# Kernel tuning notes

Hardware: AMD Instinct MI355X
Metric: run time of the kernel (lower is better)

## Reference

```python
import jax, jax.numpy as jnp
import numpy as np
from jax import lax

B, C, IC, NH, H, W, HID = 32, 128, 256, 8, 64, 64, 512


def _bn(x, g, b, m, v, eps):
    # inference-mode BatchNorm2d over NCHW
    inv = g / jnp.sqrt(v + eps)
    return x * inv[None, :, None, None] + (b - m * inv)[None, :, None, None]


def setup_inputs() -> dict:
    key = jax.random.key(0)
    ks = jax.random.split(key, 10)
    n = lambda i, shape, s: jax.random.normal(ks[i], shape, jnp.float32) * s
    return {
        "x": n(0, (B, C, H, W), 1.0),
        "bn1_g": jnp.ones((C,), jnp.float32),
        "bn1_b": jnp.zeros((C,), jnp.float32),
        "bn1_m": n(1, (C,), 0.1),
        "bn1_v": jax.random.uniform(ks[2], (C,), jnp.float32, 0.5, 1.5),
        "k": n(3, (IC, C), 0.001),   # torch.randn(...)*0.001, 1x1 kernel flattened
        "v": n(4, (C, IC), 0.001),
        "bn2_g": jnp.ones((C,), jnp.float32),
        "bn2_b": jnp.zeros((C,), jnp.float32),
        "bn2_m": n(5, (C,), 0.1),
        "bn2_v": jax.random.uniform(ks[6], (C,), jnp.float32, 0.5, 1.5),
        "w1": n(7, (HID, C, 3, 3), 0.05),
        "b1": jnp.zeros((HID,), jnp.float32),
        "w2": n(8, (C, HID, 3, 3), 0.05),
        "b2": jnp.zeros((C,), jnp.float32),
    }


def _conv3x3(x, w, b):
    y = lax.conv_general_dilated(x, w, (1, 1), 'SAME',
                                 dimension_numbers=('NCHW', 'OIHW', 'NCHW'))
    return y + b[None, :, None, None]


def reference(x, bn1_g, bn1_b, bn1_m, bn1_v, k, v,
              bn2_g, bn2_b, bn2_m, bn2_v, w1, b1, w2, b2):
    # --- ExternalAttention (use_cross_kv=False, same_in_out_chs -> stride 1) ---
    h = _bn(x, bn1_g, bn1_b, bn1_m, bn1_v, 1e-5)
    h = jnp.einsum('bchw,oc->bohw', h, k)            # 1x1 conv with external k bank
    # double normalization (_act_dn): softmax over spatial, sum-normalize per head-channel
    h = h.reshape(B, NH, IC // NH, H * W)
    h = jax.nn.softmax(h, axis=3)
    h = h / (jnp.sum(h, axis=2, keepdims=True) + 1e-6)
    h = h.reshape(B, IC, H, W)
    h = jnp.einsum('bchw,oc->bohw', h, v)            # 1x1 conv with external v bank
    x = x + h                                        # residual (EABlock wrapper)
    # --- MLP1 (BN eps=1e-6, 3x3 conv, GELU, 3x3 conv; dropout inactive in eval) ---
    m = _bn(x, bn2_g, bn2_b, bn2_m, bn2_v, 1e-6)
    m = _conv3x3(m, w1, b1)
    m = jax.nn.gelu(m, approximate=False)            # torch nn.GELU default = exact erf
    m = _conv3x3(m, w2, b2)
    return x + m
```

## Files before the change

### kernel.cpp

```cpp
#include <hip/hip_runtime.h>
#include <hip/hip_bf16.h>
#include <math.h>


#define Bn 32
#define Cn 128
#define ICn 256
#define NHn 8
#define HWn 4096
#define HIDn 512
#define GPAD 40

typedef __bf16 bf16x8 __attribute__((ext_vector_type(8)));
typedef float f32x4 __attribute__((ext_vector_type(4)));

__device__ __forceinline__ uint32_t bf16r(float v) {
  uint32_t u = __float_as_uint(v);
  return (u + 0x7FFFu + ((u >> 16) & 1u)) >> 16;
}
__device__ __forceinline__ void split_bf16(float v, uint32_t& h, uint32_t& l) {
  h = bf16r(v);
  float rem = v - __uint_as_float(h << 16);
  l = bf16r(rem);
}
__device__ __forceinline__ uint4 pack8(const float* v) {
  uint32_t w[4];
#pragma unroll
  for (int q = 0; q < 4; ++q)
    w[q] = bf16r(v[2 * q]) | (bf16r(v[2 * q + 1]) << 16);
  return make_uint4(w[0], w[1], w[2], w[3]);
}
#define MFMA(a, b, c) __builtin_amdgcn_mfma_f32_16x16x32_bf16((a), (b), (c), 0, 0, 0)

__global__ __launch_bounds__(256) void prep_a_kernel(
    const float* __restrict__ bn1_g, const float* __restrict__ bn1_b,
    const float* __restrict__ bn1_m, const float* __restrict__ bn1_v,
    const float* __restrict__ kmat,
    const float* __restrict__ bn2_g, const float* __restrict__ bn2_b,
    const float* __restrict__ bn2_m, const float* __restrict__ bn2_v,
    float* __restrict__ keff, float* __restrict__ biask,
    float* __restrict__ inv2, float* __restrict__ beta2) {
  __shared__ float sinv1[Cn], sbeta1[Cn];
  const int t = threadIdx.x;
  if (t < Cn) {
    float i1 = bn1_g[t] / sqrtf(bn1_v[t] + 1e-5f);
    sinv1[t] = i1;
    sbeta1[t] = bn1_b[t] - bn1_m[t] * i1;
    float i2 = bn2_g[t] / sqrtf(bn2_v[t] + 1e-6f);
    inv2[t] = i2;
    beta2[t] = bn2_b[t] - bn2_m[t] * i2;
  }
  __syncthreads();
  float bk = 0.f;
  for (int c = 0; c < Cn; ++c) {
    float kv = kmat[t * Cn + c];
    keff[t * Cn + c] = kv * sinv1[c];
    bk += kv * sbeta1[c];
  }
  biask[t] = bk;
}

__global__ __launch_bounds__(256) void prep_b_kernel(
    const float* __restrict__ keff, const float* __restrict__ vmat,
    const float* __restrict__ w1, const float* __restrict__ w2,
    ushort* __restrict__ k1h, ushort* __restrict__ k1l,
    ushort* __restrict__ vh, ushort* __restrict__ vl,
    ushort* __restrict__ wt1h, ushort* __restrict__ wt1l,
    ushort* __restrict__ wt2h, ushort* __restrict__ wt2l) {
  const int stride = gridDim.x * blockDim.x;
  const int tid0 = blockIdx.x * blockDim.x + threadIdx.x;
  uint32_t h, l;
  for (int d = tid0; d < ICn * Cn; d += stride) {
    int e = d & 7, lane = (d >> 3) & 63, f = d >> 9;
    int ib = f & 3, ob = f >> 2;
    int oc = ob * 16 + (lane & 15), k = ib * 32 + (lane >> 4) * 8 + e;
    split_bf16(keff[oc * Cn + k], h, l);
    k1h[d] = (ushort)h; k1l[d] = (ushort)l;
  }
  for (int d = tid0; d < Cn * ICn; d += stride) {
    int e = d & 7, lane = (d >> 3) & 63, f = d >> 9;
    int ib = f & 7, ob = f >> 3;
    int oc = ob * 16 + (lane & 15), k = ib * 32 + (lane >> 4) * 8 + e;
    split_bf16(vmat[oc * ICn + k], h, l);
    vh[d] = (ushort)h; vl[d] = (ushort)l;
  }
  for (int d = tid0; d < 9 * HIDn * Cn; d += stride) {
    int e = d & 7, lane = (d >> 3) & 63, f = d >> 9;
    int ib = f & 3, obt = f >> 2;
    int ob = obt & 31, tap = obt >> 5;
    int oc = ob * 16 + (lane & 15), k = ib * 32 + (lane >> 4) * 8 + e;
    split_bf16(w1[(oc * Cn + k) * 9 + tap], h, l);
    wt1h[d] = (ushort)h; wt1l[d] = (ushort)l;
  }
  for (int d = tid0; d < 9 * Cn * HIDn; d += stride) {
    int e = d & 7, lane = (d >> 3) & 63, f = d >> 9;
    int ib = f & 15, obt = f >> 4;
    int ob = obt & 7, tap = obt >> 3;
    int oc = ob * 16 + (lane & 15), k = ib * 32 + (lane >> 4) * 8 + e;
    split_bf16(w2[(oc * HIDn + k) * 9 + tap], h, l);
    wt2h[d] = (ushort)h; wt2l[d] = (ushort)l;
  }
}

__global__ __launch_bounds__(256, 4) void gemm1_mfma(
    const float* __restrict__ x, const ushort* __restrict__ k1h,
    const ushort* __restrict__ k1l, const float* __restrict__ biask,
    float* __restrict__ S, int b0) {
  const int tid = threadIdx.x, lane = tid & 63, wave = tid >> 6;
  const int wm = wave >> 1, wn = wave & 1;
  const int l15 = lane & 15, lg = lane >> 4;
  const int p0 = blockIdx.x * 128;
  const int oc0 = blockIdx.y * 128;
  const int bg = b0 + blockIdx.z;
  __shared__ __align__(16) ushort Xb[128 * GPAD];
  f32x4 acc[4][4] = {};
  for (int c0 = 0; c0 < Cn; c0 += 32) {
    __syncthreads();
    for (int i = tid; i < 512; i += 256) {
      int p = i & 127, g = i >> 7;
      const float* src = x + ((size_t)bg * Cn + c0 + g * 8) * HWn + p0 + p;
      float v[8];
#pragma unroll
      for (int j = 0; j < 8; ++j) v[j] = src[(size_t)j * HWn];
      *(uint4*)&Xb[p * GPAD + g * 8] = pack8(v);
    }
    __syncthreads();
    bf16x8 Bf[4];
#pragma unroll
    for (int nf = 0; nf < 4; ++nf)
      Bf[nf] = *(const bf16x8*)&Xb[(wn * 64 + nf * 16 + l15) * GPAD + lg * 8];
#pragma unroll
    for (int mf = 0; mf < 4; ++mf) {
      int fidx = ((oc0 >> 4) + wm * 4 + mf) * 4 + (c0 >> 5);
      bf16x8 Ah = *(const bf16x8*)(k1h + (size_t)fidx * 512 + lane * 8);
      bf16x8 Al = *(const bf16x8*)(k1l + (size_t)fidx * 512 + lane * 8);
#pragma unroll
      for (int nf = 0; nf < 4; ++nf)
        acc[mf][nf] = MFMA(Al, Bf[nf], MFMA(Ah, Bf[nf], acc[mf][nf]));
    }
  }
#pragma unroll
  for (int mf = 0; mf < 4; ++mf)
#pragma unroll
    for (int r = 0; r < 4; ++r) {
      int oc = oc0 + wm * 64 + mf * 16 + lg * 4 + r;
      float bk = biask[oc];
#pragma unroll
      for (int nf = 0; nf < 4; ++nf) {
        int p = p0 + wn * 64 + nf * 16 + l15;
        S[((size_t)blockIdx.z * ICn + oc) * HWn + p] = acc[mf][nf][r] + bk;
      }
    }
}

__global__ __launch_bounds__(256) void softmax_kernel(float* __restrict__ S) {
  __shared__ float row[HWn];
  __shared__ float red[4];
  const int t = threadIdx.x;
  float4* rowv = (float4*)row;
  float4* Sv = (float4*)(S + (size_t)blockIdx.x * HWn);
  float lmax = -1e30f;
#pragma unroll
  for (int i = 0; i < 4; ++i) {
    float4 v = Sv[t + 256 * i];
    rowv[t + 256 * i] = v;
    lmax = fmaxf(lmax, fmaxf(fmaxf(v.x, v.y), fmaxf(v.z, v.w)));
  }
#pragma unroll
  for (int off = 32; off; off >>= 1) lmax = fmaxf(lmax, __shfl_xor(lmax, off));
  if ((t & 63) == 0) red[t >> 6] = lmax;
  __syncthreads();
  lmax = fmaxf(fmaxf(red[0], red[1]), fmaxf(red[2], red[3]));
  float lsum = 0.f;
#pragma unroll
  for (int i = 0; i < 4; ++i) {
    float4 v = rowv[t + 256 * i];
    v.x = expf(v.x - lmax); v.y = expf(v.y - lmax);
    v.z = expf(v.z - lmax); v.w = expf(v.w - lmax);
    rowv[t + 256 * i] = v;
    lsum += v.x + v.y + v.z + v.w;
  }
#pragma unroll
  for (int off = 32; off; off >>= 1) lsum += __shfl_xor(lsum, off);
  __syncthreads();
  if ((t & 63) == 0) red[t >> 6] = lsum;
  __syncthreads();
  lsum = red[0] + red[1] + red[2] + red[3];
  float inv = 1.0f / lsum;
#pragma unroll
  for (int i = 0; i < 4; ++i) {
    float4 v = rowv[t + 256 * i];
    v.x *= inv; v.y *= inv; v.z *= inv; v.w *= inv;
    Sv[t + 256 * i] = v;
  }
}

__global__ __launch_bounds__(256) void hsum_kernel(const float* __restrict__ S,
                                                   float* __restrict__ hsum) {
  const int p4 = blockIdx.x * 256 + threadIdx.x;
  const int hh = blockIdx.y, bz = blockIdx.z;
  const float* base = S + ((size_t)bz * ICn + hh * 32) * HWn;
  float4 a = make_float4(0.f, 0.f, 0.f, 0.f);
#pragma unroll
  for (int i = 0; i < 32; ++i) {
    float4 v = ((const float4*)(base + (size_t)i * HWn))[p4];
    a.x += v.x; a.y += v.y; a.z += v.z; a.w += v.w;
  }
  ((float4*)(hsum + ((size_t)bz * NHn + hh) * HWn))[p4] = a;
}

__global__ __launch_bounds__(256, 4) void gemm2_mfma(
    const float* __restrict__ S, const ushort* __restrict__ vh,
    const ushort* __restrict__ vl, const float* __restrict__ hsum,
    const float* __restrict__ x, float* __restrict__ x2, int b0) {
  const int tid = threadIdx.x, lane = tid & 63, wave = tid >> 6;
  const int wm = wave >> 1, wn = wave & 1;
  const int l15 = lane & 15, lg = lane >> 4;
  const int p0 = blockIdx.x * 128;
  const int bz = blockIdx.z, bg = b0 + bz;
  __shared__ __align__(16) ushort Xb[128 * GPAD];
  f32x4 acc[4][4] = {};
  for (int hh = 0; hh < NHn; ++hh) {
    __syncthreads();
    for (int i = tid; i < 512; i += 256) {
      int p = i & 127, g = i >> 7;
      const float* src = S + ((size_t)bz * ICn + hh * 32 + g * 8) * HWn + p0 + p;
      float rr = 1.0f / (hsum[((size_t)bz * NHn + hh) * HWn + p0 + p] + 1e-6f);
      float v[8];
#pragma unroll
      for (int j = 0; j < 8; ++j) v[j] = src[(size_t)j * HWn] * rr;
      *(uint4*)&Xb[p * GPAD + g * 8] = pack8(v);
    }
    __syncthreads();
    bf16x8 Bf[4];
#pragma unroll
    for (int nf = 0; nf < 4; ++nf)
      Bf[nf] = *(const bf16x8*)&Xb[(wn * 64 + nf * 16 + l15) * GPAD + lg * 8];
#pragma unroll
    for (int mf = 0; mf < 4; ++mf) {
      int fidx = (wm * 4 + mf) * 8 + hh;
      bf16x8 Ah = *(const bf16x8*)(vh + (size_t)fidx * 512 + lane * 8);
      bf16x8 Al = *(const bf16x8*)(vl + (size_t)fidx * 512 + lane * 8);
#pragma unroll
      for (int nf = 0; nf < 4; ++nf)
        acc[mf][nf] = MFMA(Al, Bf[nf], MFMA(Ah, Bf[nf], acc[mf][nf]));
    }
  }
#pragma unroll
  for (int mf = 0; mf < 4; ++mf)
#pragma unroll
    for (int r = 0; r < 4; ++r) {
      int c = wm * 64 + mf * 16 + lg * 4 + r;
#pragma unroll
      for (int nf = 0; nf < 4; ++nf) {
        int p = p0 + wn * 64 + nf * 16 + l15;
        size_t off = ((size_t)bg * Cn + c) * HWn + p;
        x2[off] = x[off] + acc[mf][nf][r];
      }
    }
}

template <int IN_C, int OUT_C, bool IN_NHWC, bool DO_BN, bool GELU_NHWC,
          bool DO_RESID, bool IN_ABS, bool OUT_ABS>
__global__ __launch_bounds__(256, 4) void conv_mfma(
    const void* __restrict__ in_v, const ushort* __restrict__ wth,
    const ushort* __restrict__ wtl, const float* __restrict__ bias,
    const float* __restrict__ inv2, const float* __restrict__ beta2,
    const float* __restrict__ resid, void* __restrict__ out_v, int b0) {
  constexpr int NOB = OUT_C / 16, NIB = IN_C / 32;
  const int tid = threadIdx.x, lane = tid & 63, wave = tid >> 6;
  const int wm = wave >> 1, wn = wave & 1;
  const int l15 = lane & 15, lg = lane >> 4;
  const int p0 = blockIdx.x * 128;
  const int y0 = p0 >> 6;
  const int oc0 = blockIdx.y * 128;
  const int bz = blockIdx.z;
  const int bin = IN_ABS ? (b0 + bz) : bz;
  const int bout = OUT_ABS ? (b0 + bz) : bz;
  __shared__ __align__(16) ushort Xb[4 * 66 * GPAD];
  f32x4 acc[4][4] = {};

  for (int ic0 = 0; ic0 < IN_C; ic0 += 32) {
    __syncthreads();
    for (int i = tid; i < 4 * 66 * 4; i += 256) {
      int c = i % 66;
      int rg = i / 66;
      int r = rg & 3, g = rg >> 2;
      int gy = y0 - 1 + r, gx = c - 1;
      bool inb = (gy >= 0 && gy < 64 && gx >= 0 && gx < 64);
      uint4 w = make_uint4(0u, 0u, 0u, 0u);
      if constexpr (IN_NHWC) {
        if (inb)
          w = *(const uint4*)((const ushort*)in_v +
                              (((size_t)bin * HWn + gy * 64 + gx) * IN_C + ic0 +
                               g * 8));
      } else {
        float v[8] = {};
        if (inb) {
          const float* src = (const float*)in_v +
                             ((size_t)bin * IN_C + ic0 + g * 8) * HWn +
                             gy * 64 + gx;
#pragma unroll
          for (int j = 0; j < 8; ++j) {
            float val = src[(size_t)j * HWn];
            if constexpr (DO_BN)
              val = val * inv2[ic0 + g * 8 + j] + beta2[ic0 + g * 8 + j];
            v[j] = val;
          }
        }
        w = pack8(v);
      }
      *(uint4*)&Xb[(r * 66 + c) * GPAD + g * 8] = w;
    }
    __syncthreads();

#pragma unroll
    for (int kh = 0; kh < 3; ++kh)
#pragma unroll
      for (int kw = 0; kw < 3; ++kw) {
        const int tap = kh * 3 + kw;
        bf16x8 Bf[4];
#pragma unroll
        for (int nf = 0; nf < 4; ++nf) {
          int n = wn * 64 + nf * 16 + l15;
          int addr = (((n >> 6) + kh) * 66 + (n & 63) + kw) * GPAD + lg * 8;
          Bf[nf] = *(const bf16x8*)&Xb[addr];
        }
#pragma unroll
        for (int mf = 0; mf < 4; ++mf) {
          size_t fidx =
              ((size_t)(tap * NOB + (oc0 >> 4) + wm * 4 + mf)) * NIB +
              (ic0 >> 5);
          bf16x8 Ah = *(const bf16x8*)(wth + fidx * 512 + lane * 8);
          bf16x8 Al = *(const bf16x8*)(wtl + fidx * 512 + lane * 8);
#pragma unroll
          for (int nf = 0; nf < 4; ++nf)
            acc[mf][nf] = MFMA(Al, Bf[nf], MFMA(Ah, Bf[nf], acc[mf][nf]));
        }
      }
  }

  if constexpr (GELU_NHWC) {
#pragma unroll
    for (int mf = 0; mf < 4; ++mf) {
      int ocb = oc0 + wm * 64 + mf * 16 + lg * 4;
#pragma unroll
      for (int nf = 0; nf < 4; ++nf) {
        int n = wn * 64 + nf * 16 + l15;
        size_t pos = (size_t)bout * HWn + p0 + n;
        ushort4 pk;
        float vv;
        vv = acc[mf][nf][0] + bias[ocb + 0];
        pk.x = (ushort)bf16r(0.5f * vv * (1.f + erff(vv * 0.70710678118654752f)));
        vv = acc[mf][nf][1] + bias[ocb + 1];
        pk.y = (ushort)bf16r(0.5f * vv * (1.f + erff(vv * 0.70710678118654752f)));
        vv = acc[mf][nf][2] + bias[ocb + 2];
        pk.z = (ushort)bf16r(0.5f * vv * (1.f + erff(vv * 0.70710678118654752f)));
        vv = acc[mf][nf][3] + bias[ocb + 3];
        pk.w = (ushort)bf16r(0.5f * vv * (1.f + erff(vv * 0.70710678118654752f)));
        *(ushort4*)((ushort*)out_v + pos * OUT_C + ocb) = pk;
      }
    }
  } else {
#pragma unroll
    for (int mf = 0; mf < 4; ++mf)
#pragma unroll
      for (int r = 0; r < 4; ++r) {
        int oc = oc0 + wm * 64 + mf * 16 + lg * 4 + r;
        float bv = bias[oc];
#pragma unroll
        for (int nf = 0; nf < 4; ++nf) {
          int n = wn * 64 + nf * 16 + l15;
          size_t off = ((size_t)bout * OUT_C + oc) * HWn + p0 + n;
          float vv = acc[mf][nf][r] + bv;
          if constexpr (DO_RESID) vv += resid[off];
          ((float*)out_v)[off] = vv;
        }
      }
  }
}

extern "C" void kernel_launch(void* const* d_in, const int* in_sizes, int n_in,
                              void* d_out, int out_size, void* d_ws,
                              size_t ws_size, hipStream_t stream) {
  const float* x = (const float*)d_in[0];
  const float* bn1_g = (const float*)d_in[1];
  const float* bn1_b = (const float*)d_in[2];
  const float* bn1_m = (const float*)d_in[3];
  const float* bn1_v = (const float*)d_in[4];
  const float* kmat = (const float*)d_in[5];
  const float* vmat = (const float*)d_in[6];
  const float* bn2_g = (const float*)d_in[7];
  const float* bn2_b = (const float*)d_in[8];
  const float* bn2_m = (const float*)d_in[9];
  const float* bn2_v = (const float*)d_in[10];
  const float* w1 = (const float*)d_in[11];
  const float* b1 = (const float*)d_in[12];
  const float* w2 = (const float*)d_in[13];
  const float* b2 = (const float*)d_in[14];
  float* out = (float*)d_out;

  char* p = (char*)d_ws;
  float* keff = (float*)p;   p += (size_t)ICn * Cn * 4;
  float* biask = (float*)p;  p += 1024;
  float* inv2 = (float*)p;   p += 512;
  float* beta2 = (float*)p;  p += 512;
  ushort* k1h = (ushort*)p;  p += (size_t)ICn * Cn * 2;
  ushort* k1l = (ushort*)p;  p += (size_t)ICn * Cn * 2;
  ushort* vh = (ushort*)p;   p += (size_t)Cn * ICn * 2;
  ushort* vl = (ushort*)p;   p += (size_t)Cn * ICn * 2;
  ushort* wt1h = (ushort*)p; p += (size_t)9 * HIDn * Cn * 2;
  ushort* wt1l = (ushort*)p; p += (size_t)9 * HIDn * Cn * 2;
  ushort* wt2h = (ushort*)p; p += (size_t)9 * Cn * HIDn * 2;
  ushort* wt2l = (ushort*)p; p += (size_t)9 * Cn * HIDn * 2;
  size_t const_bytes = (size_t)(p - (char*)d_ws);

  const size_t SM_BYTES = (size_t)ICn * HWn * 4;
  const size_t HS_BYTES = (size_t)NHn * HWn * 4;
  int bc = 32;
  while (bc > 1 && const_bytes + (size_t)bc * (SM_BYTES + HS_BYTES) > ws_size)
    bc >>= 1;
  float* S = (float*)p;
  ushort* mid = (ushort*)p;
  float* hsum = (float*)(p + (size_t)bc * SM_BYTES);
  float* x2 = out;

  prep_a_kernel<<<dim3(1), dim3(256), 0, stream>>>(
      bn1_g, bn1_b, bn1_m, bn1_v, kmat, bn2_g, bn2_b, bn2_m, bn2_v, keff,
      biask, inv2, beta2);
  prep_b_kernel<<<dim3(1024), dim3(256), 0, stream>>>(
      keff, vmat, w1, w2, k1h, k1l, vh, vl, wt1h, wt1l, wt2h, wt2l);

  for (int b0 = 0; b0 < Bn; b0 += bc) {
    gemm1_mfma<<<dim3(32, 2, bc), dim3(256), 0, stream>>>(x, k1h, k1l, biask,
                                                          S, b0);
    softmax_kernel<<<dim3(bc * ICn), dim3(256), 0, stream>>>(S);
    hsum_kernel<<<dim3(4, NHn, bc), dim3(256), 0, stream>>>(S, hsum);
    gemm2_mfma<<<dim3(32, 1, bc), dim3(256), 0, stream>>>(S, vh, vl, hsum, x,
                                                          x2, b0);
    conv_mfma<Cn, HIDn, false, true, true, false, true, false>
        <<<dim3(32, 4, bc), dim3(256), 0, stream>>>(x2, wt1h, wt1l, b1, inv2,
                                                    beta2, nullptr, mid, b0);
    conv_mfma<HIDn, Cn, true, false, false, true, false, true>
        <<<dim3(32, 1, bc), dim3(256), 0, stream>>>(mid, wt2h, wt2l, b2,
                                                    nullptr, nullptr, x2, out,
                                                    b0);
  }
}
```

Before: 1.443 ms.

## Store conv mid activation in channel-paired planar layout and double-buffer weight loads

```diff
diff --git a/kernel.cpp b/kernel.cpp
--- a/kernel.cpp
+++ b/kernel.cpp
@@ -260,9 +260,9 @@
     }
 }
 
-template <int IN_C, int OUT_C, bool IN_NHWC, bool DO_BN, bool GELU_NHWC,
+template <int IN_C, int OUT_C, bool IN_PAIRED, bool DO_BN, bool GELU_PAIR,
           bool DO_RESID, bool IN_ABS, bool OUT_ABS>
-__global__ __launch_bounds__(256, 4) void conv_mfma(
+__global__ __launch_bounds__(256, 3) void conv_mfma(
     const void* __restrict__ in_v, const ushort* __restrict__ wth,
     const ushort* __restrict__ wtl, const float* __restrict__ bias,
     const float* __restrict__ inv2, const float* __restrict__ beta2,
@@ -279,6 +279,7 @@
   const int bout = OUT_ABS ? (b0 + bz) : bz;
   __shared__ __align__(16) ushort Xb[4 * 66 * GPAD];
   f32x4 acc[4][4] = {};
+  bf16x8 A0h[4], A0l[4], A1h[4], A1l[4];
 
   for (int ic0 = 0; ic0 < IN_C; ic0 += 32) {
     __syncthreads();
@@ -289,11 +290,17 @@
       int gy = y0 - 1 + r, gx = c - 1;
       bool inb = (gy >= 0 && gy < 64 && gx >= 0 && gx < 64);
       uint4 w = make_uint4(0u, 0u, 0u, 0u);
-      if constexpr (IN_NHWC) {
-        if (inb)
-          w = *(const uint4*)((const ushort*)in_v +
-                              (((size_t)bin * HWn + gy * 64 + gx) * IN_C + ic0 +
-                               g * 8));
+      if constexpr (IN_PAIRED) {
+        const uint32_t* src = (const uint32_t*)in_v +
+                              ((size_t)bin * (IN_C / 2) + (ic0 >> 1) + g * 4) *
+                                  HWn +
+                              gy * 64 + gx;
+        if (inb) {
+          w.x = src[0 * HWn];
+          w.y = src[1 * HWn];
+          w.z = src[2 * HWn];
+          w.w = src[3 * HWn];
+        }
       } else {
         float v[8] = {};
         if (inb) {
@@ -312,53 +319,62 @@
       }
       *(uint4*)&Xb[(r * 66 + c) * GPAD + g * 8] = w;
     }
-    __syncthreads();
-
-#pragma unroll
-    for (int kh = 0; kh < 3; ++kh)
-#pragma unroll
-      for (int kw = 0; kw < 3; ++kw) {
-        const int tap = kh * 3 + kw;
-        bf16x8 Bf[4];
-#pragma unroll
-        for (int nf = 0; nf < 4; ++nf) {
-          int n = wn * 64 + nf * 16 + l15;
-          int addr = (((n >> 6) + kh) * 66 + (n & 63) + kw) * GPAD + lg * 8;
-          Bf[nf] = *(const bf16x8*)&Xb[addr];
-        }
-#pragma unroll
-        for (int mf = 0; mf < 4; ++mf) {
-          size_t fidx =
-              ((size_t)(tap * NOB + (oc0 >> 4) + wm * 4 + mf)) * NIB +
-              (ic0 >> 5);
-          bf16x8 Ah = *(const bf16x8*)(wth + fidx * 512 + lane * 8);
-          bf16x8 Al = *(const bf16x8*)(wtl + fidx * 512 + lane * 8);
-#pragma unroll
-          for (int nf = 0; nf < 4; ++nf)
-            acc[mf][nf] = MFMA(Al, Bf[nf], MFMA(Ah, Bf[nf], acc[mf][nf]));
-        }
-      }
-  }
-
-  if constexpr (GELU_NHWC) {
+
+    auto loadA = [&](bf16x8* Dh, bf16x8* Dl, int tap) {
+#pragma unroll
+      for (int mf = 0; mf < 4; ++mf) {
+        size_t f =
+            ((size_t)(tap * NOB + (oc0 >> 4) + wm * 4 + mf)) * NIB + (ic0 >> 5);
+        Dh[mf] = *(const bf16x8*)(wth + f * 512 + lane * 8);
+        Dl[mf] = *(const bf16x8*)(wtl + f * 512 + lane * 8);
+      }
+    };
+    loadA(A0h, A0l, 0);
+    __syncthreads();
+
+#pragma unroll
+    for (int tap = 0; tap < 9; ++tap) {
+      bf16x8* curh = (tap & 1) ? A1h : A0h;
+      bf16x8* curl = (tap & 1) ? A1l : A0l;
+      bf16x8* nxth = (tap & 1) ? A0h : A1h;
+      bf16x8* nxtl = (tap & 1) ? A0l : A1l;
+      if (tap < 8) loadA(nxth, nxtl, tap + 1);
+      const int kh = tap / 3, kw = tap % 3;
+      bf16x8 Bf[4];
+#pragma unroll
+      for (int nf = 0; nf < 4; ++nf) {
+        int n = wn * 64 + nf * 16 + l15;
+        int addr = (((n >> 6) + kh) * 66 + (n & 63) + kw) * GPAD + lg * 8;
+        Bf[nf] = *(const bf16x8*)&Xb[addr];
+      }
+#pragma unroll
+      for (int mf = 0; mf < 4; ++mf)
+#pragma unroll
+        for (int nf = 0; nf < 4; ++nf)
+          acc[mf][nf] = MFMA(curl[mf], Bf[nf], MFMA(curh[mf], Bf[nf], acc[mf][nf]));
+    }
+  }
+
+  if constexpr (GELU_PAIR) {
+    uint32_t* outp = (uint32_t*)out_v;
 #pragma unroll
     for (int mf = 0; mf < 4; ++mf) {
       int ocb = oc0 + wm * 64 + mf * 16 + lg * 4;
 #pragma unroll
       for (int nf = 0; nf < 4; ++nf) {
         int n = wn * 64 + nf * 16 + l15;
-        size_t pos = (size_t)bout * HWn + p0 + n;
-        ushort4 pk;
-        float vv;
-        vv = acc[mf][nf][0] + bias[ocb + 0];
-        pk.x = (ushort)bf16r(0.5f * vv * (1.f + erff(vv * 0.70710678118654752f)));
-        vv = acc[mf][nf][1] + bias[ocb + 1];
-        pk.y = (ushort)bf16r(0.5f * vv * (1.f + erff(vv * 0.70710678118654752f)));
-        vv = acc[mf][nf][2] + bias[ocb + 2];
-        pk.z = (ushort)bf16r(0.5f * vv * (1.f + erff(vv * 0.70710678118654752f)));
-        vv = acc[mf][nf][3] + bias[ocb + 3];
-        pk.w = (ushort)bf16r(0.5f * vv * (1.f + erff(vv * 0.70710678118654752f)));
-        *(ushort4*)((ushort*)out_v + pos * OUT_C + ocb) = pk;
+        float g0, g1;
+        size_t base = ((size_t)bout * (OUT_C / 2) + (ocb >> 1)) * HWn + p0 + n;
+        g0 = acc[mf][nf][0] + bias[ocb + 0];
+        g0 = 0.5f * g0 * (1.f + erff(g0 * 0.70710678118654752f));
+        g1 = acc[mf][nf][1] + bias[ocb + 1];
+        g1 = 0.5f * g1 * (1.f + erff(g1 * 0.70710678118654752f));
+        outp[base] = bf16r(g0) | (bf16r(g1) << 16);
+        g0 = acc[mf][nf][2] + bias[ocb + 2];
+        g0 = 0.5f * g0 * (1.f + erff(g0 * 0.70710678118654752f));
+        g1 = acc[mf][nf][3] + bias[ocb + 3];
+        g1 = 0.5f * g1 * (1.f + erff(g1 * 0.70710678118654752f));
+        outp[base + HWn] = bf16r(g0) | (bf16r(g1) << 16);
       }
     }
   } else {
@@ -421,7 +437,7 @@
   while (bc > 1 && const_bytes + (size_t)bc * (SM_BYTES + HS_BYTES) > ws_size)
     bc >>= 1;
   float* S = (float*)p;
-  ushort* mid = (ushort*)p;
+  uint32_t* mid = (uint32_t*)p;
   float* hsum = (float*)(p + (size_t)bc * SM_BYTES);
   float* x2 = out;
 
```

Measured after the change: 1.978 ms. +37.0%, slower.
